# Optimization experiments

Hardware: AMD Instinct MI355X
Metric: run time of the kernel (lower is better)

## Reference

```python
import jax, jax.numpy as jnp
import numpy as np

CACHE_L = 64   # tokens per cache block
NHID = 512     # hidden size
TOPK = 8       # cache_k
THETA = 1.0    # cache_theta


def setup_inputs() -> dict:
    key = jax.random.key(0)
    k1, k2 = jax.random.split(key)
    T, B, N = 16, 16, 256
    query = jax.random.normal(k1, (T, 1, B, NHID), dtype=jnp.float32)
    keys = jax.random.normal(k2, (N, B, CACHE_L * NHID), dtype=jnp.float32)
    return {"query": query, "keys": keys}


def reference(query, keys):
    # query: (T, 1, B, H); keys: (N, B, L*H)
    T, Lq, B, H = query.shape
    N = keys.shape[0]
    # query.transpose(1,2).reshape(T, B, -1) -> (T, B, H) since Lq == 1
    q = jnp.transpose(query, (0, 2, 1, 3)).reshape(T, B, Lq * H)
    # keys.transpose(0,1).view(B, N, L, H)
    pooling_keys = jnp.transpose(keys, (1, 0, 2)).reshape(B, N, CACHE_L, H)
    # attention scores over every position j in every cache block n
    scores = jnp.einsum('ibh,bnjh->ijbn', q, pooling_keys)  # (T, L, B, N)
    scores = scores.max(axis=1)                              # (T, B, N)
    attention = jax.nn.softmax(THETA * scores / np.sqrt(H).astype(np.float32), axis=2)
    _, topk_indices = jax.lax.top_k(attention, TOPK)         # (T, B, k)
    topk_indices = jnp.transpose(topk_indices, (2, 0, 1))    # (k, T, B)
    return attention, topk_indices
```

## Files before the change

### kernel.cpp

```cpp
#include <hip/hip_runtime.h>
#include <hip/hip_bf16.h>
#include <math.h>

#define T_ 16
#define B_ 16
#define N_ 256
#define H_ 512
#define L_ 64
#define K_ 8
#define SCALE 0.04419417382415922f

template <int CTRL>
__device__ __forceinline__ float dpp_mov(float x) {
  return __int_as_float(
      __builtin_amdgcn_update_dpp(0, __float_as_int(x), CTRL, 0xF, 0xF, false));
}

__device__ __forceinline__ float reduce16(float v) {
  v += dpp_mov<0x111>(v);
  v += dpp_mov<0x112>(v);
  v += dpp_mov<0x114>(v);
  v += dpp_mov<0x118>(v);
  return v;
}

__global__ __launch_bounds__(256, 2) void score_kernel(
    const float* __restrict__ q, const float* __restrict__ keys,
    float* __restrict__ scores) {
  __shared__ float qs[8192];
  __shared__ float psum[4][4][4][16];

  const int bid  = blockIdx.x;
  const int b    = bid >> 6;
  const int wave = threadIdx.x >> 6;
  const int lane = threadIdx.x & 63;
  const int n    = ((bid & 63) << 2) | wave;

  {
    const int tid = threadIdx.x;
#pragma unroll
    for (int k = 0; k < 8; ++k) {
      const int flat = tid + (k << 8);
      const int c  = flat & 15;
      const int t  = (flat >> 4) & 15;
      const int ch = flat >> 8;
      const float4 v =
          *(const float4*)(q + ((size_t)t * B_ + b) * H_ + ch * 64 + c * 4);
      *(float4*)(qs + (size_t)flat * 4) = v;
    }
  }
  __syncthreads();

  const int r = lane >> 4;
  const int c = lane & 15;
  const float* __restrict__ kb =
      keys + ((size_t)n * B_ + b) * (size_t)(L_ * H_);
  const float* __restrict__ pbase = kb + (size_t)r * H_ + c * 4;

  float4 k0 = *(const float4*)(pbase + 0);
  float4 k1 = *(const float4*)(pbase + 2048);
  float4 k2 = *(const float4*)(pbase + 4096);
  float4 k3 = *(const float4*)(pbase + 6144);

#pragma unroll 1
  for (int gp = 0; gp < 4; ++gp) {
    float acc0[T_], acc1[T_], acc2[T_], acc3[T_];
#pragma unroll
    for (int t = 0; t < T_; ++t) acc0[t] = acc1[t] = acc2[t] = acc3[t] = 0.0f;

#pragma unroll 1
    for (int ch = 0; ch < 8; ++ch) {
      const int nxt = (ch < 7) ? ((gp << 13) + ((ch + 1) << 6))
                               : ((gp < 3) ? ((gp + 1) << 13) : 0);
      const float4 n0 = *(const float4*)(pbase + nxt);
      const float4 n1 = *(const float4*)(pbase + nxt + 2048);
      const float4 n2 = *(const float4*)(pbase + nxt + 4096);
      const float4 n3 = *(const float4*)(pbase + nxt + 6144);

      const float* qv = qs + (ch << 10);
#pragma unroll
      for (int t = 0; t < T_; ++t) {
        const float4 q4 = *(const float4*)(qv + (((t << 4) + c) << 2));
        acc0[t] = fmaf(k0.x, q4.x,
                  fmaf(k0.y, q4.y, fmaf(k0.z, q4.z, fmaf(k0.w, q4.w, acc0[t]))));
        acc1[t] = fmaf(k1.x, q4.x,
                  fmaf(k1.y, q4.y, fmaf(k1.z, q4.z, fmaf(k1.w, q4.w, acc1[t]))));
        acc2[t] = fmaf(k2.x, q4.x,
                  fmaf(k2.y, q4.y, fmaf(k2.z, q4.z, fmaf(k2.w, q4.w, acc2[t]))));
        acc3[t] = fmaf(k3.x, q4.x,
                  fmaf(k3.y, q4.y, fmaf(k3.z, q4.z, fmaf(k3.w, q4.w, acc3[t]))));
      }
      k0 = n0;
      k1 = n1;
      k2 = n2;
      k3 = n3;
    }

#pragma unroll
    for (int t = 0; t < T_; ++t) {
      const float s0 = reduce16(acc0[t]);
      const float s1 = reduce16(acc1[t]);
      const float s2 = reduce16(acc2[t]);
      const float s3 = reduce16(acc3[t]);
      if (c == 15)
        psum[wave][gp][r][t] = fmaxf(fmaxf(s0, s1), fmaxf(s2, s3));
    }
  }

  if (lane < 16) {
    float m = -3.4e38f;
#pragma unroll
    for (int gp = 0; gp < 4; ++gp)
#pragma unroll
      for (int g = 0; g < 4; ++g) m = fmaxf(m, psum[wave][gp][g][lane]);
    scores[(size_t)lane * (B_ * N_) + b * N_ + n] = m;
  }
}

__global__ __launch_bounds__(256) void softmax_topk_kernel(
    float* __restrict__ att, float* __restrict__ out_idx) {
  const int row  = blockIdx.x * 4 + (threadIdx.x >> 6);
  const int lane = threadIdx.x & 63;

  float* s = att + (size_t)row * N_;
  const float4 v4 = *(const float4*)(s + 4 * lane);
  const float v[4] = {v4.x, v4.y, v4.z, v4.w};

  float m = fmaxf(fmaxf(v[0], v[1]), fmaxf(v[2], v[3]));
#pragma unroll
  for (int d = 1; d < 64; d <<= 1) m = fmaxf(m, __shfl_xor(m, d));

  float p[4];
#pragma unroll
  for (int e = 0; e < 4; ++e) p[e] = expf(SCALE * (v[e] - m));

  float sum = p[0] + p[1] + p[2] + p[3];
#pragma unroll
  for (int d = 1; d < 64; d <<= 1) sum += __shfl_xor(sum, d);
  const float inv = 1.0f / sum;

  float a[4];
#pragma unroll
  for (int e = 0; e < 4; ++e) a[e] = p[e] * inv;

  *(float4*)(s + 4 * lane) = make_float4(a[0], a[1], a[2], a[3]);

  float w[4] = {a[0], a[1], a[2], a[3]};
  for (int kk = 0; kk < K_; ++kk) {
    float bv = w[0];
    int bn = 4 * lane;
#pragma unroll
    for (int e = 1; e < 4; ++e) {
      if (w[e] > bv) { bv = w[e]; bn = 4 * lane + e; }
    }
#pragma unroll
    for (int d = 1; d < 64; d <<= 1) {
      const float ov = __shfl_xor(bv, d);
      const int on = __shfl_xor(bn, d);
      if (ov > bv || (ov == bv && on < bn)) { bv = ov; bn = on; }
    }
    if (lane == 0) out_idx[kk * (T_ * B_) + row] = (float)bn;
#pragma unroll
    for (int e = 0; e < 4; ++e)
      if (4 * lane + e == bn) w[e] = -1.0f;
  }
}

extern "C" void kernel_launch(void* const* d_in, const int* in_sizes, int n_in,
                              void* d_out, int out_size, void* d_ws,
                              size_t ws_size, hipStream_t stream) {
  const float* q    = (const float*)d_in[0];
  const float* keys = (const float*)d_in[1];
  float* out = (float*)d_out;
  float* att = out;
  float* idx = out + T_ * B_ * N_;

  score_kernel<<<B_ * (N_ / 4), 256, 0, stream>>>(q, keys, att);
  softmax_topk_kernel<<<(T_ * B_) / 4, 256, 0, stream>>>(att, idx);
}
```

Before: 110.3 us.

## Fuse softmax/top-k into score kernel via last-block atomic ticket per batch

Merges the softmax and top-k pass into the score kernel. Each block takes an atomic ticket on a per-batch counter, and the last block for a batch runs softmax and top-k over that batch's 16 rows. This removes the separate second kernel and its dependency gap, but adds a memset of the counters, thread fences and a serialized tail in a few blocks.

```diff
diff --git a/kernel.cpp b/kernel.cpp
--- a/kernel.cpp
+++ b/kernel.cpp
@@ -24,11 +24,13 @@
   return v;
 }
 
-__global__ __launch_bounds__(256, 2) void score_kernel(
+__global__ __launch_bounds__(256, 2) void fused_kernel(
     const float* __restrict__ q, const float* __restrict__ keys,
-    float* __restrict__ scores) {
+    float* __restrict__ att, float* __restrict__ out_idx,
+    unsigned int* __restrict__ counters) {
   __shared__ float qs[8192];
   __shared__ float psum[4][4][4][16];
+  __shared__ unsigned int ticket_s;
 
   const int bid  = blockIdx.x;
   const int b    = bid >> 6;
@@ -113,56 +115,63 @@
     for (int gp = 0; gp < 4; ++gp)
 #pragma unroll
       for (int g = 0; g < 4; ++g) m = fmaxf(m, psum[wave][gp][g][lane]);
-    scores[(size_t)lane * (B_ * N_) + b * N_ + n] = m;
+    att[(size_t)lane * (B_ * N_) + b * N_ + n] = m;
   }
-}
 
-__global__ __launch_bounds__(256) void softmax_topk_kernel(
-    float* __restrict__ att, float* __restrict__ out_idx) {
-  const int row  = blockIdx.x * 4 + (threadIdx.x >> 6);
-  const int lane = threadIdx.x & 63;
+  __threadfence();
+  __syncthreads();
+  if (threadIdx.x == 0) ticket_s = atomicAdd(&counters[b], 1u);
+  __syncthreads();
+  if (ticket_s != 63u) return;
 
-  float* s = att + (size_t)row * N_;
-  const float4 v4 = *(const float4*)(s + 4 * lane);
-  const float v[4] = {v4.x, v4.y, v4.z, v4.w};
+  __threadfence();
 
-  float m = fmaxf(fmaxf(v[0], v[1]), fmaxf(v[2], v[3]));
+#pragma unroll 1
+  for (int tt = wave; tt < T_; tt += 4) {
+    float* s = att + ((size_t)tt * B_ + b) * N_;
+    const float4 v4 = *(const float4*)(s + 4 * lane);
+    const float v[4] = {v4.x, v4.y, v4.z, v4.w};
+
+    float m = fmaxf(fmaxf(v[0], v[1]), fmaxf(v[2], v[3]));
 #pragma unroll
-  for (int d = 1; d < 64; d <<= 1) m = fmaxf(m, __shfl_xor(m, d));
+    for (int d = 1; d < 64; d <<= 1) m = fmaxf(m, __shfl_xor(m, d));
 
-  float p[4];
+    float p[4];
 #pragma unroll
-  for (int e = 0; e < 4; ++e) p[e] = expf(SCALE * (v[e] - m));
+    for (int e = 0; e < 4; ++e) p[e] = expf(SCALE * (v[e] - m));
 
-  float sum = p[0] + p[1] + p[2] + p[3];
+    float sum = p[0] + p[1] + p[2] + p[3];
 #pragma unroll
-  for (int d = 1; d < 64; d <<= 1) sum += __shfl_xor(sum, d);
-  const float inv = 1.0f / sum;
+    for (int d = 1; d < 64; d <<= 1) sum += __shfl_xor(sum, d);
+    const float inv = 1.0f / sum;
 
-  float a[4];
+    float a[4];
 #pragma unroll
-  for (int e = 0; e < 4; ++e) a[e] = p[e] * inv;
+    for (int e = 0; e < 4; ++e) a[e] = p[e] * inv;
 
-  *(float4*)(s + 4 * lane) = make_float4(a[0], a[1], a[2], a[3]);
+    *(float4*)(s + 4 * lane) = make_float4(a[0], a[1], a[2], a[3]);
 
-  float w[4] = {a[0], a[1], a[2], a[3]};
-  for (int kk = 0; kk < K_; ++kk) {
-    float bv = w[0];
-    int bn = 4 * lane;
+    float w[4] = {a[0], a[1], a[2], a[3]};
+#pragma unroll 1
+    for (int kk = 0; kk < K_; ++kk) {
+      float bv = w[0];
+      int bn = 4 * lane;
 #pragma unroll
-    for (int e = 1; e < 4; ++e) {
-      if (w[e] > bv) { bv = w[e]; bn = 4 * lane + e; }
+      for (int e = 1; e < 4; ++e) {
+        if (w[e] > bv) { bv = w[e]; bn = 4 * lane + e; }
+      }
+#pragma unroll
+      for (int d = 1; d < 64; d <<= 1) {
+        const float ov = __shfl_xor(bv, d);
+        const int on = __shfl_xor(bn, d);
+        if (ov > bv || (ov == bv && on < bn)) { bv = ov; bn = on; }
+      }
+      if (lane == 0)
+        out_idx[kk * (T_ * B_) + tt * B_ + b] = (float)bn;
+#pragma unroll
+      for (int e = 0; e < 4; ++e)
+        if (4 * lane + e == bn) w[e] = -1.0f;
     }
-#pragma unroll
-    for (int d = 1; d < 64; d <<= 1) {
-      const float ov = __shfl_xor(bv, d);
-      const int on = __shfl_xor(bn, d);
-      if (ov > bv || (ov == bv && on < bn)) { bv = ov; bn = on; }
-    }
-    if (lane == 0) out_idx[kk * (T_ * B_) + row] = (float)bn;
-#pragma unroll
-    for (int e = 0; e < 4; ++e)
-      if (4 * lane + e == bn) w[e] = -1.0f;
   }
 }
 
@@ -174,7 +183,8 @@
   float* out = (float*)d_out;
   float* att = out;
   float* idx = out + T_ * B_ * N_;
+  unsigned int* counters = (unsigned int*)d_ws;
 
-  score_kernel<<<B_ * (N_ / 4), 256, 0, stream>>>(q, keys, att);
-  softmax_topk_kernel<<<(T_ * B_) / 4, 256, 0, stream>>>(att, idx);
+  hipMemsetAsync(counters, 0, B_ * sizeof(unsigned int), stream);
+  fused_kernel<<<B_ * (N_ / 4), 256, 0, stream>>>(q, keys, att, idx, counters);
 }
```

Result: slower. 321.3 us (+191.3%).
